# Kernel tuning notes

Hardware: AMD Instinct MI355X
Metric: run time of the kernel (lower is better)

The kernel has to match this reference:

```python
import jax, jax.numpy as jnp
import numpy as np

N = 50000       # nodes
F_IN = 256
F_OUT = 64
H = 4           # heads
DEG = 16        # avg degree (random edges per node)
NEG_SLOPE = 0.2


def setup_inputs() -> dict:
    key = jax.random.key(0)
    k_h, k_e, k_w, k_fc = jax.random.split(key, 4)
    h = jax.random.normal(k_h, (N, F_IN), dtype=jnp.float32)
    # random edges + explicit self-loops so every node has >= 1 out-edge
    e_rand = jax.random.randint(k_e, (2, N * DEG), 0, N, dtype=jnp.int64)
    loops = jnp.tile(jnp.arange(N, dtype=jnp.int64)[None, :], (2, 1))
    edge_index = jnp.concatenate([e_rand, loops], axis=1)  # [2, 850000]
    # Glorot-uniform-like scales
    s_w = np.sqrt(6.0 / (F_IN + F_OUT)).astype(np.float32)
    s_a = np.sqrt(6.0 / (2 * F_OUT + 1)).astype(np.float32)
    w = jax.random.uniform(k_w, (H, F_IN, F_OUT), jnp.float32, -s_w, s_w)
    fc = jax.random.uniform(k_fc, (H, 2 * F_OUT, 1), jnp.float32, -s_a, s_a)
    bias = jnp.zeros((F_OUT,), jnp.float32)
    return {"h": h, "edge_index": edge_index, "w": w, "fc": fc, "bias": bias}


def reference(h, edge_index, w, fc, bias):
    # GAT forward, vectorized over edges (dropout is identity at inference).
    n = h.shape[0]
    f_out = w.shape[2]
    src, dst = edge_index[0], edge_index[1]           # [E]
    h_prime = jnp.einsum('nf,hfo->hno', h, w)          # [H, N, F]
    a = fc[..., 0]                                     # [H, 2F]
    a_src, a_dst = a[:, :f_out], a[:, f_out:]          # [H, F] each
    s_src = jnp.einsum('hnf,hf->hn', h_prime, a_src)   # [H, N] score of center node
    s_dst = jnp.einsum('hnf,hf->hn', h_prime, a_dst)   # [H, N] score of neighbor
    e = jax.nn.leaky_relu(s_src[:, src] + s_dst[:, dst], NEG_SLOPE)  # [H, E]
    e = e.T                                            # [E, H]
    # segment softmax over edges grouped by source node
    seg_max = jax.ops.segment_max(e, src, num_segments=n)   # [N, H]
    ex = jnp.exp(e - seg_max[src])                           # [E, H]
    denom = jax.ops.segment_sum(ex, src, num_segments=n)    # [N, H]
    alpha = ex / denom[src]                                  # [E, H]
    # scatter-aggregate: out_i = sum_{j in N(i)} alpha_ij * Wh_j
    msgs = alpha[:, :, None] * jnp.transpose(h_prime[:, dst, :], (1, 0, 2))  # [E, H, F]
    out = jax.ops.segment_sum(msgs, src, num_segments=n)    # [N, H, F]
    return out.mean(axis=1) + bias                           # [N, F]
```

## Files before the change

kernel.cpp:

```cpp
#include <hip/hip_runtime.h>
#include <cfloat>

#define FIN 256
#define FOUT 64
#define NH 4
#define NEG_SLOPE 0.2f
#define SLOTS 64
#define BCAP 3072
#define P1T 4096

typedef __bf16 bf16x8 __attribute__((ext_vector_type(8)));
typedef float f32x4 __attribute__((ext_vector_type(4)));

__device__ __forceinline__ ushort f2bf(float f) {
    return (ushort)((__float_as_uint(f) + 0x8000u) >> 16);
}
__device__ __forceinline__ float bf2f(ushort u) {
    return __uint_as_float(((unsigned)u) << 16);
}
__device__ __forceinline__ float lrelu(float x) {
    return (x >= 0.f) ? x : NEG_SLOPE * x;
}

__global__ __launch_bounds__(256) void k0_wconv(const float* __restrict__ w,
                                                ushort* __restrict__ wt)
{
    const int g = blockIdx.x * 256 + threadIdx.x;
    const int hh  = g >> 14;
    const int rem = g & 16383;
    const int c   = rem >> 8;
    const int k   = rem & 255;
    wt[g] = f2bf(w[(((hh << 8) | k) << 6) | c]);
}

#define ASTRIDE 280
#define OSTRIDE 260
__global__ __launch_bounds__(256) void k1(
    const int* __restrict__ ei, int E, int nbuck,
    int* __restrict__ gcur, unsigned* __restrict__ barea, int p1B,
    const float* __restrict__ h, const ushort* __restrict__ wt,
    const float* __restrict__ fc, ushort* __restrict__ hp,
    float* __restrict__ s_src, float* __restrict__ s_dst, int N)
{
    __shared__ ushort lds[64 * ASTRIDE];
    const int tid = threadIdx.x;

    if ((int)blockIdx.x < p1B) {
        int* lcnt  = (int*)lds;
        int* lbase = (int*)lds + 512;
        for (int b = tid; b < nbuck; b += 256) lcnt[b] = 0;
        __syncthreads();

        const int e0 = (int)blockIdx.x * P1T;
        int s[16], d[16];
#pragma unroll
        for (int i = 0; i < 16; ++i) {
            const int e = e0 + i * 256 + tid;
            if (e < E) {
                s[i] = ei[e];
                d[i] = ei[E + e];
                atomicAdd(&lcnt[s[i] >> 7], 1);
            } else {
                s[i] = -1; d[i] = 0;
            }
        }
        __syncthreads();
        for (int b = tid; b < nbuck; b += 256) {
            const int c = lcnt[b];
            lbase[b] = c ? atomicAdd(&gcur[b * 16], c) : 0;
            lcnt[b] = 0;
        }
        __syncthreads();
#pragma unroll
        for (int i = 0; i < 16; ++i) {
            if (s[i] >= 0) {
                const int b = s[i] >> 7;
                const int r = atomicAdd(&lcnt[b], 1);
                const int pos = lbase[b] + r;
                if (pos < BCAP)
                    barea[(size_t)b * BCAP + pos] =
                        ((unsigned)(s[i] & 127) << 16) | (unsigned)d[i];
            }
        }
        return;
    }

    const int bid = (int)blockIdx.x - p1B;
    const int n0 = bid * 64;

#pragma unroll
    for (int half = 0; half < 2; ++half) {
        float4 va[8];
#pragma unroll
        for (int i = 0; i < 8; ++i) {
            const int idx = half * 2048 + i * 256 + tid;
            const int row  = idx >> 6;
            const int quad = idx & 63;
            const int n = n0 + row;
            va[i] = (n < N) ? ((const float4*)(h + (size_t)n * FIN))[quad]
                            : make_float4(0.f, 0.f, 0.f, 0.f);
        }
#pragma unroll
        for (int i = 0; i < 8; ++i) {
            const int idx = half * 2048 + i * 256 + tid;
            const int row  = idx >> 6;
            const int quad = idx & 63;
            ushort4 bv;
            bv.x = f2bf(va[i].x); bv.y = f2bf(va[i].y);
            bv.z = f2bf(va[i].z); bv.w = f2bf(va[i].w);
            *(ushort4*)&lds[row * ASTRIDE + quad * 4] = bv;
        }
    }
    __syncthreads();

    const int head = tid >> 6;
    const int lane = tid & 63;
    const int lrow = lane & 15;
    const int lq   = lane >> 4;

    const ushort* wth = wt + head * (64 * 256);

    f32x4 acc[4][4];
#pragma unroll
    for (int mt = 0; mt < 4; ++mt)
#pragma unroll
        for (int nt = 0; nt < 4; ++nt)
            acc[mt][nt] = (f32x4){0.f, 0.f, 0.f, 0.f};

#pragma unroll
    for (int kt = 0; kt < 8; ++kt) {
        const int kof = kt * 32 + lq * 8;
        bf16x8 bfr[4];
#pragma unroll
        for (int nt = 0; nt < 4; ++nt)
            bfr[nt] = *(const bf16x8*)&wth[(nt * 16 + lrow) * 256 + kof];
        bf16x8 af[4];
#pragma unroll
        for (int mt = 0; mt < 4; ++mt)
            af[mt] = *(const bf16x8*)&lds[(mt * 16 + lrow) * ASTRIDE + kof];
#pragma unroll
        for (int nt = 0; nt < 4; ++nt)
#pragma unroll
            for (int mt = 0; mt < 4; ++mt)
                acc[mt][nt] = __builtin_amdgcn_mfma_f32_16x16x32_bf16(
                    af[mt], bfr[nt], acc[mt][nt], 0, 0, 0);
    }

    float as_[4], ad_[4];
#pragma unroll
    for (int nt = 0; nt < 4; ++nt) {
        as_[nt] = fc[head * 2 * FOUT + nt * 16 + lrow];
        ad_[nt] = fc[head * 2 * FOUT + FOUT + nt * 16 + lrow];
    }
#pragma unroll
    for (int mt = 0; mt < 4; ++mt) {
        const int rbase = n0 + mt * 16 + lq * 4;
#pragma unroll
        for (int r = 0; r < 4; ++r) {
            const int n = rbase + r;
            float ps = 0.f, pd = 0.f;
#pragma unroll
            for (int nt = 0; nt < 4; ++nt) {
                const float v = acc[mt][nt][r];
                ps = fmaf(v, as_[nt], ps);
                pd = fmaf(v, ad_[nt], pd);
            }
            ps += __shfl_xor(ps, 1); pd += __shfl_xor(pd, 1);
            ps += __shfl_xor(ps, 2); pd += __shfl_xor(pd, 2);
            ps += __shfl_xor(ps, 4); pd += __shfl_xor(pd, 4);
            ps += __shfl_xor(ps, 8); pd += __shfl_xor(pd, 8);
            if (lrow == 0 && n < N) {
                s_src[(size_t)n * NH + head] = ps;
                s_dst[(size_t)n * NH + head] = pd;
            }
        }
    }

    __syncthreads();
#pragma unroll
    for (int mt = 0; mt < 4; ++mt)
#pragma unroll
        for (int r = 0; r < 4; ++r)
#pragma unroll
            for (int nt = 0; nt < 4; ++nt)
                lds[(mt * 16 + lq * 4 + r) * OSTRIDE +
                    (nt * 16 + lrow) * 4 + head] = f2bf(acc[mt][nt][r]);
    __syncthreads();
    for (int idx = tid; idx < 64 * 64; idx += 256) {
        const int row = idx >> 6;
        const int c   = idx & 63;
        const int n = n0 + row;
        if (n < N)
            *(ushort4*)&hp[(size_t)n * 256 + c * 4] =
                *(const ushort4*)&lds[row * OSTRIDE + c * 4];
    }
}

__global__ __launch_bounds__(256) void k2(
    const int* __restrict__ gcur, const unsigned* __restrict__ barea,
    ushort* __restrict__ col, int* __restrict__ cursor)
{
    __shared__ ushort colT[128 * SLOTS];
    __shared__ int cnt[128];
    const int tid = threadIdx.x;
    const int b = blockIdx.x;
    for (int i = tid; i < 128; i += 256) cnt[i] = 0;
    __syncthreads();
    int c = gcur[b * 16];
    if (c > BCAP) c = BCAP;
    for (int j = tid; j < c; j += 256) {
        const unsigned p = barea[(size_t)b * BCAP + j];
        const int sl = (int)(p >> 16);
        const int r = atomicAdd(&cnt[sl], 1);
        if (r < SLOTS) colT[sl * SLOTS + r] = (ushort)(p & 0xFFFFu);
    }
    __syncthreads();
    const size_t gbase = (size_t)b * 128 * SLOTS;
    for (int idx = tid; idx < 128 * SLOTS / 4; idx += 256)
        *(ushort4*)&col[gbase + (size_t)idx * 4] =
            *(const ushort4*)&colT[idx * 4];
    for (int i = tid; i < 128; i += 256)
        cursor[b * 128 + i] = cnt[i];
}

__global__ __launch_bounds__(256) void k_agg(
    const int* __restrict__ cursor, const ushort* __restrict__ col,
    const ushort* __restrict__ hp,
    const float* __restrict__ s_src, const float* __restrict__ s_dst,
    const float* __restrict__ bias, float* __restrict__ out, int N, int base)
{
    const int wid  = threadIdx.x >> 6;
    const int lane = threadIdx.x & 63;
    const int n    = base + blockIdx.x * 4 + wid;
    if (n >= N) return;

    const size_t start = (size_t)n * SLOTS;
    const int deg = min(cursor[n], SLOTS);
    const float4 ssn = ((const float4*)s_src)[n];
    const float4* sd4 = (const float4*)s_dst;

    float4 acc = make_float4(0.f, 0.f, 0.f, 0.f);

    int dreg = 0;
    float4 x = make_float4(-FLT_MAX, -FLT_MAX, -FLT_MAX, -FLT_MAX);
    if (lane < deg) {
        dreg = col[start + lane];
        const float4 sd = sd4[dreg];
        x.x = lrelu(ssn.x + sd.x);
        x.y = lrelu(ssn.y + sd.y);
        x.z = lrelu(ssn.z + sd.z);
        x.w = lrelu(ssn.w + sd.w);
    }
    float4 m = x;
#pragma unroll
    for (int d = 32; d; d >>= 1) {
        m.x = fmaxf(m.x, __shfl_xor(m.x, d));
        m.y = fmaxf(m.y, __shfl_xor(m.y, d));
        m.z = fmaxf(m.z, __shfl_xor(m.z, d));
        m.w = fmaxf(m.w, __shfl_xor(m.w, d));
    }
    float4 e = make_float4(0.f, 0.f, 0.f, 0.f);
    if (lane < deg) {
        e.x = __expf(x.x - m.x);
        e.y = __expf(x.y - m.y);
        e.z = __expf(x.z - m.z);
        e.w = __expf(x.w - m.w);
    }
    float4 s = e;
#pragma unroll
    for (int d = 32; d; d >>= 1) {
        s.x += __shfl_xor(s.x, d);
        s.y += __shfl_xor(s.y, d);
        s.z += __shfl_xor(s.z, d);
        s.w += __shfl_xor(s.w, d);
    }
    float4 alpha;
    alpha.x = e.x / s.x;
    alpha.y = e.y / s.y;
    alpha.z = e.z / s.z;
    alpha.w = e.w / s.w;

    const int nblk = (deg + 3) >> 2;
    for (int b = 0; b < nblk; ++b) {
        int dd[4]; float4 av[4]; ushort4 v[4];
#pragma unroll
        for (int u = 0; u < 4; ++u) {
            const int j = b * 4 + u;
            dd[u]   = __shfl(dreg, j);
            av[u].x = __shfl(alpha.x, j);
            av[u].y = __shfl(alpha.y, j);
            av[u].z = __shfl(alpha.z, j);
            av[u].w = __shfl(alpha.w, j);
        }
#pragma unroll
        for (int u = 0; u < 4; ++u)
            v[u] = *(const ushort4*)&hp[((size_t)dd[u] * FOUT + lane) * NH];
#pragma unroll
        for (int u = 0; u < 4; ++u) {
            acc.x = fmaf(av[u].x, bf2f(v[u].x), acc.x);
            acc.y = fmaf(av[u].y, bf2f(v[u].y), acc.y);
            acc.z = fmaf(av[u].z, bf2f(v[u].z), acc.z);
            acc.w = fmaf(av[u].w, bf2f(v[u].w), acc.w);
        }
    }

    out[(size_t)n * FOUT + lane] =
        (acc.x + acc.y + acc.z + acc.w) * 0.25f + bias[lane];
}

extern "C" void kernel_launch(void* const* d_in, const int* in_sizes, int n_in,
                              void* d_out, int out_size, void* d_ws, size_t ws_size,
                              hipStream_t stream)
{
    const float* h    = (const float*)d_in[0];
    const int*   ei   = (const int*)d_in[1];
    const float* w    = (const float*)d_in[2];
    const float* fc   = (const float*)d_in[3];
    const float* bias = (const float*)d_in[4];
    float* out = (float*)d_out;

    const int N = in_sizes[0] / FIN;
    const int E = in_sizes[1] / 2;
    const int nbuck = (N + 127) >> 7;

    char* ws = (char*)d_ws;
    auto take = [&](size_t bytes) {
        char* p = ws;
        ws += (bytes + 255) & ~(size_t)255;
        return p;
    };
    ushort*   wt      = (ushort*)take((size_t)NH * FIN * FOUT * sizeof(ushort));
    ushort*   h_prime = (ushort*)take((size_t)NH * N * FOUT * sizeof(ushort));
    float*    s_src   = (float*)take((size_t)NH * N * sizeof(float));
    float*    s_dst   = (float*)take((size_t)NH * N * sizeof(float));
    int*      cursor  = (int*)take((size_t)nbuck * 128 * sizeof(int));
    ushort*   col     = (ushort*)take((size_t)nbuck * 128 * SLOTS * sizeof(ushort));
    int*      gcur    = (int*)take((size_t)nbuck * 16 * sizeof(int));
    unsigned* barea   = (unsigned*)take((size_t)nbuck * BCAP * sizeof(unsigned));

    hipMemsetAsync(gcur, 0, (size_t)nbuck * 16 * sizeof(int), stream);

    k0_wconv<<<256, 256, 0, stream>>>(w, wt);

    const int p1B   = (E + P1T - 1) / P1T;
    const int gemmB = (N + 63) / 64;
    k1<<<p1B + gemmB, 256, 0, stream>>>(ei, E, nbuck, gcur, barea, p1B,
                                        h, wt, fc, h_prime, s_src, s_dst, N);

    k2<<<nbuck, 256, 0, stream>>>(gcur, barea, col, cursor);

    const int total_blocks = (N + 3) / 4;
    const int hb = total_blocks / 2;
    k_agg<<<hb, 256, 0, stream>>>(cursor, col, h_prime, s_src, s_dst,
                                  bias, out, N, 0);
    k_agg<<<total_blocks - hb, 256, 0, stream>>>(cursor, col, h_prime,
                                                 s_src, s_dst, bias, out, N, hb * 4);
}
```

Before: 142.1 us.

## Stage edge scatter through LDS for coalesced bucket writes; fold memset into wconv

The edge-bucketing blocks now prefix-scan the per-bucket counts in shared memory and stage packed edges sorted by bucket in LDS. They then write them out contiguously, so global stores to each bucket become mostly coalesced runs instead of scattered single writes. The memset of the global bucket cursors is folded into the weight-conversion kernel as extra blocks, removing one API call and launch. This costs extra LDS traffic and barriers, and it relies on bucket indices fitting in 9 bits (nbuck at most 512).

Measured after the change: 138.8 us. 2.4% less time.

```diff
diff --git a/kernel.cpp b/kernel.cpp
--- a/kernel.cpp
+++ b/kernel.cpp
@@ -23,14 +23,20 @@
 }
 
 __global__ __launch_bounds__(256) void k0_wconv(const float* __restrict__ w,
-                                                ushort* __restrict__ wt)
-{
-    const int g = blockIdx.x * 256 + threadIdx.x;
-    const int hh  = g >> 14;
-    const int rem = g & 16383;
-    const int c   = rem >> 8;
-    const int k   = rem & 255;
-    wt[g] = f2bf(w[(((hh << 8) | k) << 6) | c]);
+                                                ushort* __restrict__ wt,
+                                                int* __restrict__ gcur, int gn)
+{
+    if ((int)blockIdx.x < 256) {
+        const int g = blockIdx.x * 256 + threadIdx.x;
+        const int hh  = g >> 14;
+        const int rem = g & 16383;
+        const int c   = rem >> 8;
+        const int k   = rem & 255;
+        wt[g] = f2bf(w[(((hh << 8) | k) << 6) | c]);
+    } else {
+        const int g = ((int)blockIdx.x - 256) * 256 + threadIdx.x;
+        if (g < gn) gcur[g] = 0;
+    }
 }
 
 #define ASTRIDE 280
@@ -46,12 +52,16 @@
     const int tid = threadIdx.x;
 
     if ((int)blockIdx.x < p1B) {
-        int* lcnt  = (int*)lds;
-        int* lbase = (int*)lds + 512;
-        for (int b = tid; b < nbuck; b += 256) lcnt[b] = 0;
+        int* lcnt        = (int*)lds;
+        int* lscan       = lcnt + 512;
+        int* lbase       = lscan + 512;
+        unsigned* ledges = (unsigned*)(lbase + 512);
+
+        for (int b = tid; b < 512; b += 256) lcnt[b] = 0;
         __syncthreads();
 
         const int e0 = (int)blockIdx.x * P1T;
+        const int cnt_total = min(P1T, E - e0);
         int s[16], d[16];
 #pragma unroll
         for (int i = 0; i < 16; ++i) {
@@ -65,22 +75,49 @@
             }
         }
         __syncthreads();
+
+        if (tid < 64) {
+            int vals[8], sum = 0;
+#pragma unroll
+            for (int k = 0; k < 8; ++k) { vals[k] = lcnt[tid * 8 + k]; sum += vals[k]; }
+            int x = sum;
+#pragma unroll
+            for (int dd = 1; dd < 64; dd <<= 1) {
+                const int t = __shfl_up(x, dd);
+                if (tid >= dd) x += t;
+            }
+            int run = x - sum;
+#pragma unroll
+            for (int k = 0; k < 8; ++k) { lscan[tid * 8 + k] = run; run += vals[k]; }
+        }
+        __syncthreads();
+
         for (int b = tid; b < nbuck; b += 256) {
             const int c = lcnt[b];
             lbase[b] = c ? atomicAdd(&gcur[b * 16], c) : 0;
-            lcnt[b] = 0;
-        }
-        __syncthreads();
+        }
+        __syncthreads();
+        for (int b = tid; b < 512; b += 256) lcnt[b] = 0;
+        __syncthreads();
+
 #pragma unroll
         for (int i = 0; i < 16; ++i) {
             if (s[i] >= 0) {
                 const int b = s[i] >> 7;
                 const int r = atomicAdd(&lcnt[b], 1);
-                const int pos = lbase[b] + r;
-                if (pos < BCAP)
-                    barea[(size_t)b * BCAP + pos] =
-                        ((unsigned)(s[i] & 127) << 16) | (unsigned)d[i];
-            }
+                ledges[lscan[b] + r] =
+                    ((unsigned)b << 23) | ((unsigned)(s[i] & 127) << 16) |
+                    (unsigned)d[i];
+            }
+        }
+        __syncthreads();
+
+        for (int j = tid; j < cnt_total; j += 256) {
+            const unsigned p = ledges[j];
+            const int b = (int)(p >> 23);
+            const int pos = lbase[b] + (j - lscan[b]);
+            if (pos < BCAP)
+                barea[(size_t)b * BCAP + pos] = p & 0x007FFFFFu;
         }
         return;
     }
@@ -338,9 +375,8 @@
     int*      gcur    = (int*)take((size_t)nbuck * 16 * sizeof(int));
     unsigned* barea   = (unsigned*)take((size_t)nbuck * BCAP * sizeof(unsigned));
 
-    hipMemsetAsync(gcur, 0, (size_t)nbuck * 16 * sizeof(int), stream);
-
-    k0_wconv<<<256, 256, 0, stream>>>(w, wt);
+    const int gn = nbuck * 16;
+    k0_wconv<<<256 + (gn + 255) / 256, 256, 0, stream>>>(w, wt, gcur, gn);
 
     const int p1B   = (E + P1T - 1) / P1T;
     const int gemmB = (N + 63) / 64;
```
